# Optimization experiments

Measured on AMD Instinct MI355X. Metric: run time of the kernel, lower is better.

## Reference

```python
import jax, jax.numpy as jnp
import numpy as np

B, L, HID = 2, 2048, 2560
H, HKV, DH = 32, 8, 128
G = H // HKV  # GQA groups = 4
EPS = 1e-6
THETA = 1000000.0


def setup_inputs() -> dict:
    key = jax.random.key(0)
    ks = jax.random.split(key, 6)
    x = jax.random.normal(ks[0], (B, L, HID), dtype=jnp.float32)
    Wq = jax.random.normal(ks[1], (HID, H * DH), dtype=jnp.float32) * 0.02
    Wk = jax.random.normal(ks[2], (HID, HKV * DH), dtype=jnp.float32) * 0.02
    Wv = jax.random.normal(ks[3], (HID, HKV * DH), dtype=jnp.float32) * 0.02
    Wo = jax.random.normal(ks[4], (H * DH, HID), dtype=jnp.float32) * 0.02
    q_norm_w = jnp.ones((DH,), dtype=jnp.float32)
    k_norm_w = jnp.ones((DH,), dtype=jnp.float32)
    # RoPE tables, theta=1e6, non-interleaved (half-split) layout
    inv_freq = 1.0 / (THETA ** (jnp.arange(0, DH, 2, dtype=jnp.float32) / DH))
    pos = jnp.arange(L, dtype=jnp.float32)
    freqs = pos[:, None] * inv_freq[None, :]              # [L, DH/2]
    emb = jnp.concatenate([freqs, freqs], axis=-1)        # [L, DH]
    cos = jnp.broadcast_to(jnp.cos(emb)[None], (B, L, DH))
    sin = jnp.broadcast_to(jnp.sin(emb)[None], (B, L, DH))
    return {"x": x, "Wq": Wq, "Wk": Wk, "Wv": Wv, "Wo": Wo,
            "q_norm_w": q_norm_w, "k_norm_w": k_norm_w,
            "cos": cos, "sin": sin}


def _rmsnorm(x, w):
    xf = x.astype(jnp.float32)
    var = jnp.mean(xf * xf, axis=-1, keepdims=True)
    return (xf * jax.lax.rsqrt(var + EPS)).astype(x.dtype) * w


def _rotate_half(x):
    x1, x2 = jnp.split(x, 2, axis=-1)
    return jnp.concatenate([-x2, x1], axis=-1)


def reference(x, Wq, Wk, Wv, Wo, q_norm_w, k_norm_w, cos, sin):
    b, l, _ = x.shape
    q = (x @ Wq).reshape(b, l, H, DH)
    k = (x @ Wk).reshape(b, l, HKV, DH)
    v = (x @ Wv).reshape(b, l, HKV, DH).transpose(0, 2, 1, 3)   # [B,HKV,L,DH]
    q = _rmsnorm(q, q_norm_w).transpose(0, 2, 1, 3)             # [B,H,L,DH]
    k = _rmsnorm(k, k_norm_w).transpose(0, 2, 1, 3)             # [B,HKV,L,DH]
    c = cos[:, None]  # [B,1,L,DH]
    s = sin[:, None]
    q = q * c + _rotate_half(q) * s
    k = k * c + _rotate_half(k) * s
    # GQA SDPA, causal
    qg = q.reshape(b, HKV, G, l, DH)
    scale = 1.0 / np.sqrt(DH)
    scores = jnp.einsum('bkgqd,bkmd->bkgqm', qg, k) * scale     # [B,HKV,G,L,L]
    causal = jnp.tril(jnp.ones((l, l), dtype=bool))
    scores = jnp.where(causal, scores, jnp.finfo(scores.dtype).min)
    attn = jax.nn.softmax(scores, axis=-1)
    out = jnp.einsum('bkgqm,bkmd->bkgqd', attn, v)              # [B,HKV,G,L,DH]
    out = out.reshape(b, H, l, DH).transpose(0, 2, 1, 3).reshape(b, l, H * DH)
    return out @ Wo
```

## Files before the change

### kernel.cpp

```cpp
#include <hip/hip_runtime.h>

typedef unsigned short u16;
typedef unsigned int u32;
using bf16x8 = __attribute__((ext_vector_type(8))) __bf16;
using f32x4  = __attribute__((ext_vector_type(4))) float;

typedef const void __attribute__((address_space(1)))* gas1p;
typedef void __attribute__((address_space(3)))* las3p;

__device__ __forceinline__ void gload16(const void* g, void* l) {
  __builtin_amdgcn_global_load_lds((gas1p)g, (las3p)l, 16, 0, 0);
}

__device__ __forceinline__ u16 f2bf(float f) {
  union { float f; unsigned u; } v; v.f = f;
  unsigned r = v.u + 0x7FFFu + ((v.u >> 16) & 1u);
  return (u16)(r >> 16);
}
__device__ __forceinline__ float bf2f(u16 h) {
  union { unsigned u; float f; } v; v.u = ((unsigned)h) << 16;
  return v.f;
}

__global__ __launch_bounds__(256)
void cvt_f32_bf16(const float4* __restrict__ in, uint2* __restrict__ out, int n4) {
  int i = blockIdx.x * 256 + threadIdx.x;
  if (i >= n4) return;
  float4 v = in[i];
  uint2 o;
  o.x = (unsigned)f2bf(v.x) | ((unsigned)f2bf(v.y) << 16);
  o.y = (unsigned)f2bf(v.z) | ((unsigned)f2bf(v.w) << 16);
  out[i] = o;
}

__global__ __launch_bounds__(256)
void transpose_w(const float* __restrict__ in, u16* __restrict__ out, int R, int C) {
  __shared__ float tile[32][33];
  const int tx = threadIdx.x & 31, ty = threadIdx.x >> 5;
  const int r0 = blockIdx.y * 32, c0 = blockIdx.x * 32;
#pragma unroll
  for (int i = 0; i < 4; i++)
    tile[ty + i * 8][tx] = in[(size_t)(r0 + ty + i * 8) * C + c0 + tx];
  __syncthreads();
#pragma unroll
  for (int i = 0; i < 4; i++)
    out[(size_t)(c0 + ty + i * 8) * R + r0 + tx] = f2bf(tile[tx][ty + i * 8]);
}

__global__ __launch_bounds__(256)
void transpose_v(const u16* __restrict__ QKV, u16* __restrict__ Vt) {
  __shared__ u16 tile[32][34];
  const int tx = threadIdx.x & 31, ty = threadIdx.x >> 5;
  const int l0 = blockIdx.x * 32, d0 = blockIdx.y * 32;
  const int bkv = blockIdx.z;
  const int b = bkv >> 3, kvh = bkv & 7;
#pragma unroll
  for (int i = 0; i < 4; i++)
    tile[ty + i * 8][tx] =
        QKV[(size_t)(b * 2048 + l0 + ty + i * 8) * 6144 + 5120 + kvh * 128 + d0 + tx];
  __syncthreads();
#pragma unroll
  for (int i = 0; i < 4; i++)
    Vt[((size_t)bkv * 128 + d0 + ty + i * 8) * 2048 + l0 + tx] = tile[tx][ty + i * 8];
}

__global__ __launch_bounds__(256)
void norm_rope(const u16* __restrict__ QKV, const float* __restrict__ qw,
               const float* __restrict__ kw, const float* __restrict__ cosp,
               const float* __restrict__ sinp, u16* __restrict__ Qr,
               u16* __restrict__ Kr) {
  const int rid = blockIdx.x * 4 + (threadIdx.x >> 6);
  const int lane = threadIdx.x & 63;
  const int head = rid % 40;
  const int bl = rid / 40;
  const int b = bl >> 11, l = bl & 2047;
  const u16* src; const float* w; u16* dst; float scale;
  if (head < 32) {
    src = QKV + (size_t)bl * 6144 + head * 128;
    w = qw;
    dst = Qr + ((size_t)(b * 32 + head) * 2048 + l) * 128;
    scale = 0.08838834764831845f;
  } else {
    const int kvh = head - 32;
    src = QKV + (size_t)bl * 6144 + 4096 + kvh * 128;
    w = kw;
    dst = Kr + ((size_t)(b * 8 + kvh) * 2048 + l) * 128;
    scale = 1.0f;
  }
  float lo = bf2f(src[lane]);
  float hi = bf2f(src[lane + 64]);
  float ss = lo * lo + hi * hi;
#pragma unroll
  for (int m = 1; m < 64; m <<= 1) ss += __shfl_xor(ss, m, 64);
  const float rstd = rsqrtf(ss * (1.0f / 128.0f) + 1e-6f) * scale;
  const float nlo = lo * rstd * w[lane];
  const float nhi = hi * rstd * w[lane + 64];
  const float* cb = cosp + (size_t)bl * 128;
  const float* sb = sinp + (size_t)bl * 128;
  dst[lane]      = f2bf(nlo * cb[lane]      - nhi * sb[lane]);
  dst[lane + 64] = f2bf(nhi * cb[lane + 64] + nlo * sb[lane + 64]);
}

#define BAR __builtin_amdgcn_s_barrier()
#define WLG { asm volatile("s_waitcnt lgkmcnt(0)" ::: "memory");            \
              __builtin_amdgcn_sched_barrier(0); }
#define WVMn(n) asm volatile("s_waitcnt vmcnt(" #n ")" ::: "memory")
#define SP1 __builtin_amdgcn_s_setprio(1)
#define SP0 __builtin_amdgcn_s_setprio(0)

template <int MINW, int BM, int BN, int WM, int WN, typename CT>
__global__ __launch_bounds__(512, MINW)
void gemmT(const u16* __restrict__ A, const u16* __restrict__ Bt,
           CT* __restrict__ C, int N, int K, int MT) {
  extern __shared__ char smem[];
  constexpr int ASZ = BM * 128;
  constexpr int BSZ = BN * 128;
  constexpr int MI = BM / WM / 16;
  constexpr int NJF = BN / WN / 16;
  constexpr int NL = BM / 64 + (BN + 63) / 64;
  const int tid = threadIdx.x, lane = tid & 63, wid = tid >> 6;
  const int wm = wid / WN, wn = wid % WN;
  const int fr = lane & 15, fq = lane >> 4;
  const int qx = (int)gridDim.x >> 3;
  const int wg = ((int)blockIdx.x & 7) * qx + ((int)blockIdx.x >> 3);
  const int bx = wg / MT, by = wg - bx * MT;
  const int m0 = by * BM, n0 = bx * BN;
  const u16* Ab = A + (size_t)m0 * K;
  const u16* Bb = Bt + (size_t)n0 * K;

#define ABUF(c) (smem + (c) * ASZ)
#define BBUF(c) (smem + 2 * ASZ + (c) * BSZ)

  f32x4 acc[MI][NJF];
#pragma unroll
  for (int i = 0; i < MI; i++)
#pragma unroll
    for (int j = 0; j < NJF; j++)
#pragma unroll
      for (int r = 0; r < 4; r++) acc[i][j][r] = 0.f;

  auto stage = [&](int c, int kk) {
#pragma unroll
    for (int l = 0; l < BM / 64; l++) {
      const int u = tid + 512 * l, row = u >> 3, ch = u & 7;
      gload16(Ab + (size_t)row * K + ((ch ^ (row & 7)) << 3) + kk,
              ABUF(c) + (u << 4));
    }
#pragma unroll
    for (int l = 0; l < BN / 64; l++) {
      const int u = tid + 512 * l, row = u >> 3, ch = u & 7;
      gload16(Bb + (size_t)row * K + ((ch ^ (row & 7)) << 3) + kk,
              BBUF(c) + (u << 4));
    }
    if constexpr ((BN % 64) != 0) {
      const int u = (BN / 64) * 512 + (tid & 255), row = u >> 3, ch = u & 7;
      gload16(Bb + (size_t)row * K + ((ch ^ (row & 7)) << 3) + kk,
              BBUF(c) + (u << 4));
    }
  };

  const int NT = K >> 6;
  stage(0, 0);
  stage(1, 64);
  if constexpr (NL == 5) { WVMn(5); } else { WVMn(7); }
  BAR;

  bf16x8 af[MI][2], bf[NJF][2];
  for (int t = 0; t < NT; t++) {
    const int c = t & 1;
#pragma unroll
    for (int i = 0; i < MI; i++) {
      const int row = (wm * MI + i) * 16 + fr;
#pragma unroll
      for (int ks = 0; ks < 2; ks++)
        af[i][ks] = *(const bf16x8*)(ABUF(c) + row * 128 +
                                     ((((ks << 2) + fq) ^ (row & 7)) << 4));
    }
#pragma unroll
    for (int j = 0; j < NJF; j++) {
      const int row = (j * WN + wn) * 16 + fr;
#pragma unroll
      for (int ks = 0; ks < 2; ks++)
        bf[j][ks] = *(const bf16x8*)(BBUF(c) + row * 128 +
                                     ((((ks << 2) + fq) ^ (row & 7)) << 4));
    }
    WLG;
    BAR;
    int t2 = t + 2; if (t2 >= NT) t2 -= NT;
    stage(c, t2 << 6);
    if constexpr (NL == 5) { WVMn(5); } else { WVMn(7); }
    SP1;
#pragma unroll
    for (int j = 0; j < NJF; j++)
#pragma unroll
      for (int i = 0; i < MI; i++) {
        acc[i][j] = __builtin_amdgcn_mfma_f32_16x16x32_bf16(af[i][0], bf[j][0],
                                                            acc[i][j], 0, 0, 0);
        acc[i][j] = __builtin_amdgcn_mfma_f32_16x16x32_bf16(af[i][1], bf[j][1],
                                                            acc[i][j], 0, 0, 0);
      }
    SP0;
    BAR;
  }
  WVMn(0);

#pragma unroll
  for (int i = 0; i < MI; i++) {
    const int row0 = m0 + (wm * MI + i) * 16 + fq * 4;
#pragma unroll
    for (int j = 0; j < NJF; j++) {
      const int col = n0 + (j * WN + wn) * 16 + fr;
#pragma unroll
      for (int r = 0; r < 4; r++) {
        const size_t idx = (size_t)(row0 + r) * N + col;
        if constexpr (sizeof(CT) == 2) C[idx] = f2bf(acc[i][j][r]);
        else C[idx] = acc[i][j][r];
      }
    }
  }
#undef ABUF
#undef BBUF
}

__global__ __launch_bounds__(256, 2)
void attn_fwd(const u16* __restrict__ Qr, const u16* __restrict__ Kr,
              const u16* __restrict__ Vt, u16* __restrict__ AO) {
  const int L = 2048, DH = 128;
  __shared__ u16 Ks[2][64 * 128];
  __shared__ u16 Vs[2][128 * 64];
  const int tid = threadIdx.x, lane = tid & 63, wid = tid >> 6;
  const int fr = lane & 15, fq = lane >> 4;
  const int j = blockIdx.x >> 4;
  const int grp = blockIdx.x & 15;
  const int kvh = grp >> 1, b = grp & 1;
  const int h = kvh * 4 + wid;

  const u16* Kbase = Kr + (size_t)(b * 8 + kvh) * L * DH;
  const u16* Vbase = Vt + (size_t)(b * 8 + kvh) * DH * L;

  int Dly[4], kOff[4], vOff[4];
#pragma unroll
  for (int p = 0; p < 4; p++) {
    const int D = (tid + p * 256) * 16;
    Dly[p] = D;
    const int kr = D >> 8, kc = ((D >> 4) & 15) ^ (kr & 7);
    kOff[p] = kr * 128 + kc * 8;
    const int vr = D >> 7, vc = ((D >> 4) & 7) ^ (vr & 7);
    vOff[p] = vr * 2048 + vc * 8;
  }

  const bool B5 = (lane & 32) != 0;
  const bool A4 = (lane & 16) != 0;

  auto stage = [&](int kt, int bufi) {
    const int k0 = kt * 64;
#pragma unroll
    for (int p = 0; p < 4; p++) {
      gload16(Kbase + (size_t)k0 * 128 + kOff[p], (char*)&Ks[bufi][0] + Dly[p]);
      gload16(Vbase + k0 + vOff[p], (char*)&Vs[bufi][0] + Dly[p]);
    }
  };

  for (int half = 0; half < 2; half++) {
    const int t = half ? 63 - j : j;
    const int nk = (t >> 1) + 1;

    bf16x8 qf[2][4];
#pragma unroll
    for (int g = 0; g < 2; g++) {
      const int qq = t * 32 + g * 16 + fr;
      const u16* qbase = Qr + ((size_t)(b * 32 + h) * L + qq) * DH + fq * 8;
#pragma unroll
      for (int dt = 0; dt < 4; dt++) qf[g][dt] = *(const bf16x8*)(qbase + dt * 32);
    }
    asm volatile("s_waitcnt vmcnt(0)" ::: "memory");

    f32x4 o[2][8];
#pragma unroll
    for (int g = 0; g < 2; g++)
#pragma unroll
      for (int d = 0; d < 8; d++)
#pragma unroll
        for (int r = 0; r < 4; r++) o[g][d][r] = 0.f;
    float mrow[2] = {-__builtin_huge_valf(), -__builtin_huge_valf()};
    float lrow[2] = {0.f, 0.f};

    __builtin_amdgcn_s_barrier();
    stage(0, 0);
    int cur = 0;

    for (int kt = 0; kt < nk; kt++) {
      if (kt + 1 < nk) {
        stage(kt + 1, cur ^ 1);
        asm volatile("s_waitcnt vmcnt(8)" ::: "memory");
      } else {
        asm volatile("s_waitcnt vmcnt(0)" ::: "memory");
      }
      __builtin_amdgcn_s_barrier();

      const u16* KsB = &Ks[cur][0];
      const u16* VsB = &Vs[cur][0];
      const int k0 = kt * 64;

      f32x4 s4[2][4];
#pragma unroll
      for (int g = 0; g < 2; g++)
#pragma unroll
        for (int ni = 0; ni < 4; ni++)
#pragma unroll
          for (int r = 0; r < 4; r++) s4[g][ni][r] = 0.f;
#pragma unroll
      for (int ni = 0; ni < 4; ni++) {
        const int krow = ni * 16 + fr;
        const int sw = (krow & 7) << 4;
#pragma unroll
        for (int dt = 0; dt < 4; dt++) {
          const int off = (krow * 256 + dt * 64 + fq * 16) ^ sw;
          bf16x8 kf = *(const bf16x8*)((const char*)KsB + off);
          s4[0][ni] = __builtin_amdgcn_mfma_f32_16x16x32_bf16(kf, qf[0][dt], s4[0][ni], 0, 0, 0);
          s4[1][ni] = __builtin_amdgcn_mfma_f32_16x16x32_bf16(kf, qf[1][dt], s4[1][ni], 0, 0, 0);
        }
      }

      if (kt == nk - 1) {
#pragma unroll
        for (int g = 0; g < 2; g++) {
          const int qq = t * 32 + g * 16 + fr;
#pragma unroll
          for (int ni = 0; ni < 4; ni++)
#pragma unroll
            for (int r = 0; r < 4; r++)
              if (k0 + ni * 16 + fq * 4 + r > qq) s4[g][ni][r] = -1e30f;
        }
      }

      bf16x8 pb[2][2];
#pragma unroll
      for (int g = 0; g < 2; g++) {
        float mt = s4[g][0][0];
#pragma unroll
        for (int ni = 0; ni < 4; ni++)
#pragma unroll
          for (int r = 0; r < 4; r++) mt = fmaxf(mt, s4[g][ni][r]);
        mt = fmaxf(mt, __shfl_xor(mt, 16, 64));
        mt = fmaxf(mt, __shfl_xor(mt, 32, 64));

        if (!__all(mt <= mrow[g] + 8.f)) {
          const float mn = fmaxf(mrow[g], mt);
          const float corr = exp2f((mrow[g] - mn) * 1.44269504f);
          mrow[g] = mn;
          lrow[g] *= corr;
#pragma unroll
          for (int d = 0; d < 8; d++)
#pragma unroll
            for (int r = 0; r < 4; r++) o[g][d][r] *= corr;
        }

        const float ml = mrow[g] * 1.44269504f;
        float rs = 0.f;
#pragma unroll
        for (int ni = 0; ni < 4; ni++)
#pragma unroll
          for (int r = 0; r < 4; r++) {
            const float pv = exp2f(fmaf(s4[g][ni][r], 1.44269504f, -ml));
            s4[g][ni][r] = pv;
            rs += pv;
          }
        rs += __shfl_xor(rs, 16, 64);
        rs += __shfl_xor(rs, 32, 64);
        lrow[g] += rs;

        u32 pk[4][2];
#pragma unroll
        for (int ni = 0; ni < 4; ni++) {
          pk[ni][0] = __builtin_amdgcn_perm(__float_as_uint(s4[g][ni][1]),
                                            __float_as_uint(s4[g][ni][0]), 0x07060302u);
          pk[ni][1] = __builtin_amdgcn_perm(__float_as_uint(s4[g][ni][3]),
                                            __float_as_uint(s4[g][ni][2]), 0x07060302u);
        }
#pragma unroll
        for (int ks = 0; ks < 2; ks++) {
          u32 r00 = pk[2 * ks + 0][0], r01 = pk[2 * ks + 0][1];
          u32 r10 = pk[2 * ks + 1][0], r11 = pk[2 * ks + 1][1];
          u32 e0 = __shfl_xor(B5 ? r00 : r10, 32, 64);
          u32 t00 = B5 ? e0 : r00, t10 = B5 ? r10 : e0;
          u32 e1 = __shfl_xor(B5 ? r01 : r11, 32, 64);
          u32 t01 = B5 ? e1 : r01, t11 = B5 ? r11 : e1;
          u32 e2 = __shfl_xor(A4 ? t00 : t10, 16, 64);
          u32 u00 = A4 ? e2 : t00, u10 = A4 ? t10 : e2;
          u32 e3 = __shfl_xor(A4 ? t01 : t11, 16, 64);
          u32 u01 = A4 ? e3 : t01, u11 = A4 ? t11 : e3;
          union { u32 u[4]; bf16x8 v; } pbv;
          pbv.u[0] = u00; pbv.u[1] = u01; pbv.u[2] = u10; pbv.u[3] = u11;
          pb[g][ks] = pbv.v;
        }
      }

#pragma unroll
      for (int d = 0; d < 8; d++) {
        const int vrow = d * 16 + fr;
        const int sw = (vrow & 7) << 4;
#pragma unroll
        for (int ks = 0; ks < 2; ks++) {
          const int off = (vrow * 128 + ks * 64 + fq * 16) ^ sw;
          bf16x8 vf = *(const bf16x8*)((const char*)VsB + off);
          o[0][d] = __builtin_amdgcn_mfma_f32_16x16x32_bf16(vf, pb[0][ks], o[0][d], 0, 0, 0);
          o[1][d] = __builtin_amdgcn_mfma_f32_16x16x32_bf16(vf, pb[1][ks], o[1][d], 0, 0, 0);
        }
      }
      __builtin_amdgcn_s_barrier();
      cur ^= 1;
    }

#pragma unroll
    for (int g = 0; g < 2; g++) {
      const float inv = 1.f / lrow[g];
      const int qq = t * 32 + g * 16 + fr;
      u16* obase = AO + ((size_t)b * L + qq) * 4096 + h * 128 + fq * 4;
#pragma unroll
      for (int d = 0; d < 8; d++) {
        uint2 w;
        w.x = (u32)f2bf(o[g][d][0] * inv) | ((u32)f2bf(o[g][d][1] * inv) << 16);
        w.y = (u32)f2bf(o[g][d][2] * inv) | ((u32)f2bf(o[g][d][3] * inv) << 16);
        *(uint2*)(obase + d * 16) = w;
      }
    }
  }
}

extern "C" void kernel_launch(void* const* d_in, const int* in_sizes, int n_in,
                              void* d_out, int out_size, void* d_ws, size_t ws_size,
                              hipStream_t stream) {
  const float* x    = (const float*)d_in[0];
  const float* Wq   = (const float*)d_in[1];
  const float* Wk   = (const float*)d_in[2];
  const float* Wv   = (const float*)d_in[3];
  const float* Wo   = (const float*)d_in[4];
  const float* qw   = (const float*)d_in[5];
  const float* kw   = (const float*)d_in[6];
  const float* cosp = (const float*)d_in[7];
  const float* sinp = (const float*)d_in[8];
  float* out = (float*)d_out;
  char* ws = (char*)d_ws;

  u16* xb    = (u16*)(ws);
  u16* WqkvT = (u16*)(ws + 20971520);
  u16* WoT   = (u16*)(ws + 52428800);
  u16* QKV   = (u16*)(ws + 73400320);
  u16* AO    = QKV;
  u16* Qrr   = (u16*)(ws + 123731968);
  u16* Krr   = (u16*)(ws + 157286400);
  u16* Vtt   = (u16*)(ws + 165675008);

  hipFuncSetAttribute(reinterpret_cast<const void*>(&gemmT<4, 128, 192, 2, 4, u16>),
                      hipFuncAttributeMaxDynamicSharedMemorySize, 81920);
  hipFuncSetAttribute(reinterpret_cast<const void*>(&gemmT<2, 256, 160, 4, 2, float>),
                      hipFuncAttributeMaxDynamicSharedMemorySize, 106496);

  cvt_f32_bf16<<<10240, 256, 0, stream>>>((const float4*)x, (uint2*)xb, 2621440);
  transpose_w<<<dim3(128, 80), 256, 0, stream>>>(Wq, WqkvT, 2560, 4096);
  transpose_w<<<dim3(32, 80), 256, 0, stream>>>(Wk, WqkvT + (size_t)4096 * 2560, 2560, 1024);
  transpose_w<<<dim3(32, 80), 256, 0, stream>>>(Wv, WqkvT + (size_t)5120 * 2560, 2560, 1024);
  transpose_w<<<dim3(80, 128), 256, 0, stream>>>(Wo, WoT, 4096, 2560);

  gemmT<4, 128, 192, 2, 4, u16><<<1024, 512, 81920, stream>>>(xb, WqkvT, QKV, 6144, 2560, 32);

  norm_rope<<<40960, 256, 0, stream>>>(QKV, qw, kw, cosp, sinp, Qrr, Krr);
  transpose_v<<<dim3(64, 4, 16), 256, 0, stream>>>(QKV, Vtt);

  attn_fwd<<<dim3(512), 256, 0, stream>>>(Qrr, Krr, Vtt, AO);

  gemmT<2, 256, 160, 4, 2, float><<<256, 512, 106496, stream>>>(AO, WoT, out, 2560, 4096, 16);
}
```

Measured before the change: 418.8 us.

## Split attention into one block per q-tile, single-buffer V, raise occupancy

The attention kernel no longer pairs a light and a heavy causal q-tile per block. It launches 1024 blocks, one per 32-row tile, scheduled heaviest first (t = 63 - blockIdx/16). V is now single-buffered and its next tile is loaded after the PV step, while K stays double-buffered. This cuts shared memory so launch bounds can request 3 blocks per CU. The aim is better latency hiding and load balance, at the cost of tighter register limits, which may cause spills, and less overlap for the V load.

```diff
diff --git a/kernel.cpp b/kernel.cpp
--- a/kernel.cpp
+++ b/kernel.cpp
@@ -222,18 +222,19 @@
 #undef BBUF
 }
 
-__global__ __launch_bounds__(256, 2)
+__global__ __launch_bounds__(256, 3)
 void attn_fwd(const u16* __restrict__ Qr, const u16* __restrict__ Kr,
               const u16* __restrict__ Vt, u16* __restrict__ AO) {
   const int L = 2048, DH = 128;
   __shared__ u16 Ks[2][64 * 128];
-  __shared__ u16 Vs[2][128 * 64];
+  __shared__ u16 Vs[128 * 64];
   const int tid = threadIdx.x, lane = tid & 63, wid = tid >> 6;
   const int fr = lane & 15, fq = lane >> 4;
-  const int j = blockIdx.x >> 4;
+  const int t = 63 - (int)(blockIdx.x >> 4);
   const int grp = blockIdx.x & 15;
   const int kvh = grp >> 1, b = grp & 1;
   const int h = kvh * 4 + wid;
+  const int nk = (t >> 1) + 1;
 
   const u16* Kbase = Kr + (size_t)(b * 8 + kvh) * L * DH;
   const u16* Vbase = Vt + (size_t)(b * 8 + kvh) * DH * L;
@@ -252,178 +253,182 @@
   const bool B5 = (lane & 32) != 0;
   const bool A4 = (lane & 16) != 0;
 
-  auto stage = [&](int kt, int bufi) {
+  auto stageK = [&](int kt, int bufi) {
     const int k0 = kt * 64;
 #pragma unroll
-    for (int p = 0; p < 4; p++) {
+    for (int p = 0; p < 4; p++)
       gload16(Kbase + (size_t)k0 * 128 + kOff[p], (char*)&Ks[bufi][0] + Dly[p]);
-      gload16(Vbase + k0 + vOff[p], (char*)&Vs[bufi][0] + Dly[p]);
-    }
   };
-
-  for (int half = 0; half < 2; half++) {
-    const int t = half ? 63 - j : j;
-    const int nk = (t >> 1) + 1;
-
-    bf16x8 qf[2][4];
+  auto stageV = [&](int kt) {
+    const int k0 = kt * 64;
+#pragma unroll
+    for (int p = 0; p < 4; p++)
+      gload16(Vbase + k0 + vOff[p], (char*)&Vs[0] + Dly[p]);
+  };
+
+  bf16x8 qf[2][4];
+#pragma unroll
+  for (int g = 0; g < 2; g++) {
+    const int qq = t * 32 + g * 16 + fr;
+    const u16* qbase = Qr + ((size_t)(b * 32 + h) * L + qq) * DH + fq * 8;
+#pragma unroll
+    for (int dt = 0; dt < 4; dt++) qf[g][dt] = *(const bf16x8*)(qbase + dt * 32);
+  }
+  asm volatile("s_waitcnt vmcnt(0)" ::: "memory");
+
+  f32x4 o[2][8];
+#pragma unroll
+  for (int g = 0; g < 2; g++)
+#pragma unroll
+    for (int d = 0; d < 8; d++)
+#pragma unroll
+      for (int r = 0; r < 4; r++) o[g][d][r] = 0.f;
+  float mrow[2] = {-__builtin_huge_valf(), -__builtin_huge_valf()};
+  float lrow[2] = {0.f, 0.f};
+
+  stageK(0, 0);
+  stageV(0);
+  asm volatile("s_waitcnt vmcnt(4)" ::: "memory");
+  __builtin_amdgcn_s_barrier();
+  int cur = 0;
+
+  for (int kt = 0; kt < nk; kt++) {
+    if (kt + 1 < nk) stageK(kt + 1, cur ^ 1);
+
+    const u16* KsB = &Ks[cur][0];
+    const int k0 = kt * 64;
+
+    f32x4 s4[2][4];
+#pragma unroll
+    for (int g = 0; g < 2; g++)
+#pragma unroll
+      for (int ni = 0; ni < 4; ni++)
+#pragma unroll
+        for (int r = 0; r < 4; r++) s4[g][ni][r] = 0.f;
+#pragma unroll
+    for (int ni = 0; ni < 4; ni++) {
+      const int krow = ni * 16 + fr;
+      const int sw = (krow & 7) << 4;
+#pragma unroll
+      for (int dt = 0; dt < 4; dt++) {
+        const int off = (krow * 256 + dt * 64 + fq * 16) ^ sw;
+        bf16x8 kf = *(const bf16x8*)((const char*)KsB + off);
+        s4[0][ni] = __builtin_amdgcn_mfma_f32_16x16x32_bf16(kf, qf[0][dt], s4[0][ni], 0, 0, 0);
+        s4[1][ni] = __builtin_amdgcn_mfma_f32_16x16x32_bf16(kf, qf[1][dt], s4[1][ni], 0, 0, 0);
+      }
+    }
+
+    if (kt == nk - 1) {
+#pragma unroll
+      for (int g = 0; g < 2; g++) {
+        const int qq = t * 32 + g * 16 + fr;
+#pragma unroll
+        for (int ni = 0; ni < 4; ni++)
+#pragma unroll
+          for (int r = 0; r < 4; r++)
+            if (k0 + ni * 16 + fq * 4 + r > qq) s4[g][ni][r] = -1e30f;
+      }
+    }
+
+    bf16x8 pb[2][2];
 #pragma unroll
     for (int g = 0; g < 2; g++) {
-      const int qq = t * 32 + g * 16 + fr;
-      const u16* qbase = Qr + ((size_t)(b * 32 + h) * L + qq) * DH + fq * 8;
-#pragma unroll
-      for (int dt = 0; dt < 4; dt++) qf[g][dt] = *(const bf16x8*)(qbase + dt * 32);
-    }
+      float mt = s4[g][0][0];
+#pragma unroll
+      for (int ni = 0; ni < 4; ni++)
+#pragma unroll
+        for (int r = 0; r < 4; r++) mt = fmaxf(mt, s4[g][ni][r]);
+      mt = fmaxf(mt, __shfl_xor(mt, 16, 64));
+      mt = fmaxf(mt, __shfl_xor(mt, 32, 64));
+
+      if (!__all(mt <= mrow[g] + 8.f)) {
+        const float mn = fmaxf(mrow[g], mt);
+        const float corr = exp2f((mrow[g] - mn) * 1.44269504f);
+        mrow[g] = mn;
+        lrow[g] *= corr;
+#pragma unroll
+        for (int d = 0; d < 8; d++)
+#pragma unroll
+          for (int r = 0; r < 4; r++) o[g][d][r] *= corr;
+      }
+
+      const float ml = mrow[g] * 1.44269504f;
+      float rs = 0.f;
+#pragma unroll
+      for (int ni = 0; ni < 4; ni++)
+#pragma unroll
+        for (int r = 0; r < 4; r++) {
+          const float pv = exp2f(fmaf(s4[g][ni][r], 1.44269504f, -ml));
+          s4[g][ni][r] = pv;
+          rs += pv;
+        }
+      rs += __shfl_xor(rs, 16, 64);
+      rs += __shfl_xor(rs, 32, 64);
+      lrow[g] += rs;
+
+      u32 pk[4][2];
+#pragma unroll
+      for (int ni = 0; ni < 4; ni++) {
+        pk[ni][0] = __builtin_amdgcn_perm(__float_as_uint(s4[g][ni][1]),
+                                          __float_as_uint(s4[g][ni][0]), 0x07060302u);
+        pk[ni][1] = __builtin_amdgcn_perm(__float_as_uint(s4[g][ni][3]),
+                                          __float_as_uint(s4[g][ni][2]), 0x07060302u);
+      }
+#pragma unroll
+      for (int ks = 0; ks < 2; ks++) {
+        u32 r00 = pk[2 * ks + 0][0], r01 = pk[2 * ks + 0][1];
+        u32 r10 = pk[2 * ks + 1][0], r11 = pk[2 * ks + 1][1];
+        u32 e0 = __shfl_xor(B5 ? r00 : r10, 32, 64);
+        u32 t00 = B5 ? e0 : r00, t10 = B5 ? r10 : e0;
+        u32 e1 = __shfl_xor(B5 ? r01 : r11, 32, 64);
+        u32 t01 = B5 ? e1 : r01, t11 = B5 ? r11 : e1;
+        u32 e2 = __shfl_xor(A4 ? t00 : t10, 16, 64);
+        u32 u00 = A4 ? e2 : t00, u10 = A4 ? t10 : e2;
+        u32 e3 = __shfl_xor(A4 ? t01 : t11, 16, 64);
+        u32 u01 = A4 ? e3 : t01, u11 = A4 ? t11 : e3;
+        union { u32 u[4]; bf16x8 v; } pbv;
+        pbv.u[0] = u00; pbv.u[1] = u01; pbv.u[2] = u10; pbv.u[3] = u11;
+        pb[g][ks] = pbv.v;
+      }
+    }
+
+    if (kt + 1 < nk) {
+      asm volatile("s_waitcnt vmcnt(4)" ::: "memory");
+    } else {
+      asm volatile("s_waitcnt vmcnt(0)" ::: "memory");
+    }
+    __builtin_amdgcn_s_barrier();
+
+#pragma unroll
+    for (int d = 0; d < 8; d++) {
+      const int vrow = d * 16 + fr;
+      const int sw = (vrow & 7) << 4;
+#pragma unroll
+      for (int ks = 0; ks < 2; ks++) {
+        const int off = (vrow * 128 + ks * 64 + fq * 16) ^ sw;
+        bf16x8 vf = *(const bf16x8*)((const char*)Vs + off);
+        o[0][d] = __builtin_amdgcn_mfma_f32_16x16x32_bf16(vf, pb[0][ks], o[0][d], 0, 0, 0);
+        o[1][d] = __builtin_amdgcn_mfma_f32_16x16x32_bf16(vf, pb[1][ks], o[1][d], 0, 0, 0);
+      }
+    }
+
     asm volatile("s_waitcnt vmcnt(0)" ::: "memory");
-
-    f32x4 o[2][8];
-#pragma unroll
-    for (int g = 0; g < 2; g++)
-#pragma unroll
-      for (int d = 0; d < 8; d++)
-#pragma unroll
-        for (int r = 0; r < 4; r++) o[g][d][r] = 0.f;
-    float mrow[2] = {-__builtin_huge_valf(), -__builtin_huge_valf()};
-    float lrow[2] = {0.f, 0.f};
-
     __builtin_amdgcn_s_barrier();
-    stage(0, 0);
-    int cur = 0;
-
-    for (int kt = 0; kt < nk; kt++) {
-      if (kt + 1 < nk) {
-        stage(kt + 1, cur ^ 1);
-        asm volatile("s_waitcnt vmcnt(8)" ::: "memory");
-      } else {
-        asm volatile("s_waitcnt vmcnt(0)" ::: "memory");
-      }
-      __builtin_amdgcn_s_barrier();
-
-      const u16* KsB = &Ks[cur][0];
-      const u16* VsB = &Vs[cur][0];
-      const int k0 = kt * 64;
-
-      f32x4 s4[2][4];
-#pragma unroll
-      for (int g = 0; g < 2; g++)
-#pragma unroll
-        for (int ni = 0; ni < 4; ni++)
-#pragma unroll
-          for (int r = 0; r < 4; r++) s4[g][ni][r] = 0.f;
-#pragma unroll
-      for (int ni = 0; ni < 4; ni++) {
-        const int krow = ni * 16 + fr;
-        const int sw = (krow & 7) << 4;
-#pragma unroll
-        for (int dt = 0; dt < 4; dt++) {
-          const int off = (krow * 256 + dt * 64 + fq * 16) ^ sw;
-          bf16x8 kf = *(const bf16x8*)((const char*)KsB + off);
-          s4[0][ni] = __builtin_amdgcn_mfma_f32_16x16x32_bf16(kf, qf[0][dt], s4[0][ni], 0, 0, 0);
-          s4[1][ni] = __builtin_amdgcn_mfma_f32_16x16x32_bf16(kf, qf[1][dt], s4[1][ni], 0, 0, 0);
-        }
-      }
-
-      if (kt == nk - 1) {
-#pragma unroll
-        for (int g = 0; g < 2; g++) {
-          const int qq = t * 32 + g * 16 + fr;
-#pragma unroll
-          for (int ni = 0; ni < 4; ni++)
-#pragma unroll
-            for (int r = 0; r < 4; r++)
-              if (k0 + ni * 16 + fq * 4 + r > qq) s4[g][ni][r] = -1e30f;
-        }
-      }
-
-      bf16x8 pb[2][2];
-#pragma unroll
-      for (int g = 0; g < 2; g++) {
-        float mt = s4[g][0][0];
-#pragma unroll
-        for (int ni = 0; ni < 4; ni++)
-#pragma unroll
-          for (int r = 0; r < 4; r++) mt = fmaxf(mt, s4[g][ni][r]);
-        mt = fmaxf(mt, __shfl_xor(mt, 16, 64));
-        mt = fmaxf(mt, __shfl_xor(mt, 32, 64));
-
-        if (!__all(mt <= mrow[g] + 8.f)) {
-          const float mn = fmaxf(mrow[g], mt);
-          const float corr = exp2f((mrow[g] - mn) * 1.44269504f);
-          mrow[g] = mn;
-          lrow[g] *= corr;
-#pragma unroll
-          for (int d = 0; d < 8; d++)
-#pragma unroll
-            for (int r = 0; r < 4; r++) o[g][d][r] *= corr;
-        }
-
-        const float ml = mrow[g] * 1.44269504f;
-        float rs = 0.f;
-#pragma unroll
-        for (int ni = 0; ni < 4; ni++)
-#pragma unroll
-          for (int r = 0; r < 4; r++) {
-            const float pv = exp2f(fmaf(s4[g][ni][r], 1.44269504f, -ml));
-            s4[g][ni][r] = pv;
-            rs += pv;
-          }
-        rs += __shfl_xor(rs, 16, 64);
-        rs += __shfl_xor(rs, 32, 64);
-        lrow[g] += rs;
-
-        u32 pk[4][2];
-#pragma unroll
-        for (int ni = 0; ni < 4; ni++) {
-          pk[ni][0] = __builtin_amdgcn_perm(__float_as_uint(s4[g][ni][1]),
-                                            __float_as_uint(s4[g][ni][0]), 0x07060302u);
-          pk[ni][1] = __builtin_amdgcn_perm(__float_as_uint(s4[g][ni][3]),
-                                            __float_as_uint(s4[g][ni][2]), 0x07060302u);
-        }
-#pragma unroll
-        for (int ks = 0; ks < 2; ks++) {
-          u32 r00 = pk[2 * ks + 0][0], r01 = pk[2 * ks + 0][1];
-          u32 r10 = pk[2 * ks + 1][0], r11 = pk[2 * ks + 1][1];
-          u32 e0 = __shfl_xor(B5 ? r00 : r10, 32, 64);
-          u32 t00 = B5 ? e0 : r00, t10 = B5 ? r10 : e0;
-          u32 e1 = __shfl_xor(B5 ? r01 : r11, 32, 64);
-          u32 t01 = B5 ? e1 : r01, t11 = B5 ? r11 : e1;
-          u32 e2 = __shfl_xor(A4 ? t00 : t10, 16, 64);
-          u32 u00 = A4 ? e2 : t00, u10 = A4 ? t10 : e2;
-          u32 e3 = __shfl_xor(A4 ? t01 : t11, 16, 64);
-          u32 u01 = A4 ? e3 : t01, u11 = A4 ? t11 : e3;
-          union { u32 u[4]; bf16x8 v; } pbv;
-          pbv.u[0] = u00; pbv.u[1] = u01; pbv.u[2] = u10; pbv.u[3] = u11;
-          pb[g][ks] = pbv.v;
-        }
-      }
-
-#pragma unroll
-      for (int d = 0; d < 8; d++) {
-        const int vrow = d * 16 + fr;
-        const int sw = (vrow & 7) << 4;
-#pragma unroll
-        for (int ks = 0; ks < 2; ks++) {
-          const int off = (vrow * 128 + ks * 64 + fq * 16) ^ sw;
-          bf16x8 vf = *(const bf16x8*)((const char*)VsB + off);
-          o[0][d] = __builtin_amdgcn_mfma_f32_16x16x32_bf16(vf, pb[0][ks], o[0][d], 0, 0, 0);
-          o[1][d] = __builtin_amdgcn_mfma_f32_16x16x32_bf16(vf, pb[1][ks], o[1][d], 0, 0, 0);
-        }
-      }
-      __builtin_amdgcn_s_barrier();
-      cur ^= 1;
-    }
-
-#pragma unroll
-    for (int g = 0; g < 2; g++) {
-      const float inv = 1.f / lrow[g];
-      const int qq = t * 32 + g * 16 + fr;
-      u16* obase = AO + ((size_t)b * L + qq) * 4096 + h * 128 + fq * 4;
-#pragma unroll
-      for (int d = 0; d < 8; d++) {
-        uint2 w;
-        w.x = (u32)f2bf(o[g][d][0] * inv) | ((u32)f2bf(o[g][d][1] * inv) << 16);
-        w.y = (u32)f2bf(o[g][d][2] * inv) | ((u32)f2bf(o[g][d][3] * inv) << 16);
-        *(uint2*)(obase + d * 16) = w;
-      }
+    if (kt + 1 < nk) stageV(kt + 1);
+    cur ^= 1;
+  }
+
+#pragma unroll
+  for (int g = 0; g < 2; g++) {
+    const float inv = 1.f / lrow[g];
+    const int qq = t * 32 + g * 16 + fr;
+    u16* obase = AO + ((size_t)b * L + qq) * 4096 + h * 128 + fq * 4;
+#pragma unroll
+    for (int d = 0; d < 8; d++) {
+      uint2 w;
+      w.x = (u32)f2bf(o[g][d][0] * inv) | ((u32)f2bf(o[g][d][1] * inv) << 16);
+      w.y = (u32)f2bf(o[g][d][2] * inv) | ((u32)f2bf(o[g][d][3] * inv) << 16);
+      *(uint2*)(obase + d * 16) = w;
     }
   }
 }
@@ -468,7 +473,7 @@
   norm_rope<<<40960, 256, 0, stream>>>(QKV, qw, kw, cosp, sinp, Qrr, Krr);
   transpose_v<<<dim3(64, 4, 16), 256, 0, stream>>>(QKV, Vtt);
 
-  attn_fwd<<<dim3(512), 256, 0, stream>>>(Qrr, Krr, Vtt, AO);
+  attn_fwd<<<dim3(1024), 256, 0, stream>>>(Qrr, Krr, Vtt, AO);
 
   gemmT<2, 256, 160, 4, 2, float><<<256, 512, 106496, stream>>>(AO, WoT, out, 2560, 4096, 16);
 }
```

Result: slower. 471.7 us (+12.6%).
